# Performance work log

Measured on AMD Instinct MI355X. Metric: run time of the kernel, lower is better.

Reference implementation:

```python
import jax, jax.numpy as jnp
import numpy as np

T_V = 0.1
T_Q = 0.1
NEG_VIDEO_IOU = 0.5
POS_VIDEO_TOPK = 1
MARGIN = 0.0
EPS = 1e-12


def _normalize(x):
    # F.normalize(dim=-1) with eps clamp
    n = jnp.linalg.norm(x, axis=-1, keepdims=True)
    return x / jnp.maximum(n, EPS)


def _log_cross_entropy(pos_score, all_score, neg_mask, t, m):
    pos_exp = jnp.exp((pos_score - m) / t)
    neg_exp_sum = jnp.sum(jnp.exp(all_score / t) * neg_mask, axis=-1)
    loss = -((pos_score - m) / t - jnp.log(pos_exp + neg_exp_sum))
    return jnp.mean(loss)


def setup_inputs() -> dict:
    B, C, N, S = 32, 256, 64, 64
    key = jax.random.key(0)
    k1, k2, k3 = jax.random.split(key, 3)
    video_feats = jax.random.normal(k1, (B, C, N, N), dtype=jnp.float32)
    sents_feats = jax.random.normal(k2, (S, C), dtype=jnp.float32)
    iou2ds = jax.random.uniform(k3, (S, N, N), dtype=jnp.float32)
    mask2d = jnp.triu(jnp.ones((N, N), dtype=bool))  # P = N*(N+1)/2 = 2080
    num_targets = jnp.full((B,), S // B, dtype=jnp.int32)  # sums to S
    return {"video_feats": video_feats, "sents_feats": sents_feats,
            "num_targets": num_targets, "iou2ds": iou2ds, "mask2d": mask2d}


def reference(video_feats, sents_feats, num_targets, iou2ds, mask2d):
    B, C, N, _ = video_feats.shape
    S = sents_feats.shape[0]
    K = POS_VIDEO_TOPK
    # mask2d / num_targets are structural constants -> resolve on host
    flat_idx = np.nonzero(np.asarray(mask2d).reshape(-1))[0]   # [P]
    P = flat_idx.shape[0]
    scatter_idx = np.repeat(np.arange(B), np.asarray(num_targets))  # [S]

    # masked_select of valid proposals
    vf = video_feats.reshape(B, C, N * N)[:, :, flat_idx]      # [B,C,P]
    vf = jnp.transpose(vf, (0, 2, 1))                          # [B,P,C]
    iou = iou2ds.reshape(S, N * N)[:, flat_idx]                # [S,P]

    vf = _normalize(vf)
    sf = _normalize(sents_feats)                               # [S,C]

    # top-k proposals per sentence
    topk_idx = jax.lax.top_k(iou, K)[1]                        # [S,K]
    sv = vf[scatter_idx]                                       # [S,P,C]
    topk_video = jnp.take_along_axis(sv, topk_idx[:, :, None], axis=1)  # [S,K,C]

    # inter-video loss
    inter_video_pos = jnp.einsum('skc,sc->sk', topk_video, sf)          # [S,K]
    inter_video_all = jnp.einsum('skc,tc->skt', topk_video, sf)         # [S,K,S]
    inter_video_neg_mask = (~jnp.eye(S, dtype=bool))[:, None, :]        # [S,1,S]
    loss_inter_video = _log_cross_entropy(
        inter_video_pos, inter_video_all, inter_video_neg_mask, T_V, MARGIN)

    # inter-query loss
    inter_query_all = jnp.einsum('sc,bpc->sbp', sf, vf).reshape(S, 1, B * P)
    same_video = jnp.asarray(scatter_idx)[:, None] == jnp.arange(B)[None, :]  # [S,B]
    pos_mask = same_video[:, :, None] & (iou > NEG_VIDEO_IOU)[:, None, :]     # [S,B,P]
    inter_query_neg_mask = (~pos_mask).reshape(S, 1, B * P)
    loss_inter_query = _log_cross_entropy(
        inter_video_pos, inter_query_all, inter_query_neg_mask, T_Q, MARGIN)

    return (loss_inter_video, loss_inter_query)
```

## Files before the change

### kernel.cpp

```cpp
#include <hip/hip_runtime.h>
#include <hip/hip_bf16.h>
#include <math.h>

constexpr int B_ = 32;
constexpr int C_ = 256;
constexpr int N_ = 64;
constexpr int S_ = 64;
constexpr int NPIX = N_ * N_;
constexpr int QB = B_ * N_;

#define T_V_INV 10.0f
#define T_Q_INV 10.0f
#define NEG_IOU 0.5f

typedef __attribute__((ext_vector_type(8))) short short8;
typedef __attribute__((ext_vector_type(4))) float f32x4;

static __device__ __forceinline__ unsigned short f2bf(float x) {
  __hip_bfloat16 h = __float2bfloat16(x);
  unsigned short u;
  __builtin_memcpy(&u, &h, sizeof(u));
  return u;
}

__global__ __launch_bounds__(256) void k_setup(
    const float* __restrict__ sents, const float* __restrict__ iou,
    const int* __restrict__ nt,
    float* __restrict__ sf_t, unsigned short* __restrict__ sf_frag,
    int* __restrict__ scatter, int* __restrict__ top_pix) {
  int bid = blockIdx.x, tid = threadIdx.x;
  __shared__ float wsum[4];
  __shared__ float bval[256];
  __shared__ int bidx[256];

  if (bid < S_) {
    int s = bid, c = tid;
    float v = sents[s * C_ + c];
    float ss = v * v;
    #pragma unroll
    for (int o = 32; o; o >>= 1) ss += __shfl_xor(ss, o);
    if ((c & 63) == 0) wsum[c >> 6] = ss;
    __syncthreads();
    float tot = wsum[0] + wsum[1] + wsum[2] + wsum[3];
    float rn = 1.0f / fmaxf(sqrtf(tot), 1e-12f);
    float o = v * rn;
    sf_t[c * S_ + s] = o;
    int ks = c >> 5, q = (c >> 3) & 3, j = c & 7;
    int mt = s >> 4, m = s & 15;
    sf_frag[((ks * 4 + mt) * 64 + (q * 16 + m)) * 8 + j] = f2bf(o);

    float bv = -1.0f;
    int bi = 0x7fffffff;
    for (int pix = tid; pix < NPIX; pix += 256) {
      int r = pix >> 6, c0 = pix & 63;
      if (c0 >= r) {
        float x = iou[s * NPIX + pix];
        if (x > bv) { bv = x; bi = pix; }
      }
    }
    bval[tid] = bv; bidx[tid] = bi;
    __syncthreads();
    for (int st = 128; st; st >>= 1) {
      if (tid < st) {
        float ov = bval[tid + st]; int oi = bidx[tid + st];
        if (ov > bval[tid] || (ov == bval[tid] && oi < bidx[tid])) {
          bval[tid] = ov; bidx[tid] = oi;
        }
      }
      __syncthreads();
    }
    if (tid == 0) top_pix[s] = bidx[0];
  } else {
    if (tid < S_) {
      int cum = 0, res = 0;
      for (int b = 0; b < B_; b++) {
        int nb = nt[b];
        if (tid >= cum && tid < cum + nb) res = b;
        cum += nb;
      }
      scatter[tid] = res;
    }
  }
}

__global__ __launch_bounds__(256) void k_main(
    const float* __restrict__ V, const float* __restrict__ iou,
    const short8* __restrict__ Afrag, const float* __restrict__ sf_t,
    const int* __restrict__ scatter, const int* __restrict__ top_pix,
    float* __restrict__ partials, float* __restrict__ pos_score,
    float* __restrict__ loss_vid) {
  __shared__ int ssc[S_];
  __shared__ float part[4][S_];
  __shared__ float vh[C_];
  __shared__ float red[4];
  __shared__ float pdm[4][S_];

  int tid = threadIdx.x;

  if (blockIdx.x < QB) {
    if (tid < S_) ssc[tid] = scatter[tid];
    __syncthreads();

    int b = blockIdx.x >> 6, r = blockIdx.x & 63;
    int w = tid >> 6, lane = tid & 63;
    int n = lane & 15, q = lane >> 4;
    int col = w * 16 + n;
    int pix = r * 64 + col;
    bool active = (col >= r);

    const float* vb = V + (size_t)b * C_ * NPIX + pix;
    f32x4 acc[4] = {f32x4{0,0,0,0}, f32x4{0,0,0,0}, f32x4{0,0,0,0}, f32x4{0,0,0,0}};
    float ssq = 0.0f;

    for (int ks = 0; ks < 8; ks++) {
      short8 bfrag;
      #pragma unroll
      for (int j = 0; j < 8; j++) {
        int c = ks * 32 + q * 8 + j;
        float v = active ? vb[(size_t)c * NPIX] : 0.0f;
        ssq = fmaf(v, v, ssq);
        bfrag[j] = (short)f2bf(v);
      }
      #pragma unroll
      for (int mt = 0; mt < 4; mt++) {
        short8 a = Afrag[(ks * 4 + mt) * 64 + lane];
        acc[mt] = __builtin_amdgcn_mfma_f32_16x16x32_bf16(a, bfrag, acc[mt], 0, 0, 0);
      }
    }

    ssq += __shfl_xor(ssq, 16);
    ssq += __shfl_xor(ssq, 32);
    float rs = T_Q_INV / fmaxf(sqrtf(ssq), 1e-12f);

    #pragma unroll
    for (int mt = 0; mt < 4; mt++) {
      #pragma unroll
      for (int rr = 0; rr < 4; rr++) {
        int s = mt * 16 + q * 4 + rr;
        float e = active ? __expf(acc[mt][rr] * rs) : 0.0f;
        if (active && ssc[s] == b) {
          if (iou[s * NPIX + pix] > NEG_IOU) e = 0.0f;
        }
        e += __shfl_xor(e, 1);
        e += __shfl_xor(e, 2);
        e += __shfl_xor(e, 4);
        e += __shfl_xor(e, 8);
        if (n == 0) part[w][s] = e;
      }
    }
    __syncthreads();
    if (tid < S_) {
      partials[(size_t)blockIdx.x * S_ + tid] =
          part[0][tid] + part[1][tid] + part[2][tid] + part[3][tid];
    }
  } else {
    int s = blockIdx.x - QB;
    int b = scatter[s];
    int pix = top_pix[s];
    float v = V[((size_t)b * C_ + tid) * NPIX + pix];
    float ss = v * v;
    #pragma unroll
    for (int o = 32; o; o >>= 1) ss += __shfl_xor(ss, o);
    if ((tid & 63) == 0) red[tid >> 6] = ss;
    __syncthreads();
    float tot = red[0] + red[1] + red[2] + red[3];
    float rn = 1.0f / fmaxf(sqrtf(tot), 1e-12f);
    vh[tid] = v * rn;
    __syncthreads();
    int so = tid & 63, chunk = tid >> 6;
    float pd = 0.0f;
    #pragma unroll 8
    for (int c = chunk * 64; c < chunk * 64 + 64; c++)
      pd = fmaf(vh[c], sf_t[c * S_ + so], pd);
    pdm[chunk][so] = pd;
    __syncthreads();
    if (tid < S_) {
      float dot = pdm[0][tid] + pdm[1][tid] + pdm[2][tid] + pdm[3][tid];
      if (tid == s) pos_score[s] = dot;
      float pos = __shfl(dot, s);
      float e = (tid == s) ? 0.0f : __expf(dot * T_V_INV);
      #pragma unroll
      for (int o = 32; o; o >>= 1) e += __shfl_xor(e, o);
      if (tid == 0) {
        float pp = pos * T_V_INV;
        loss_vid[s] = -(pp - logf(__expf(pp) + e));
      }
    }
  }
}

__global__ __launch_bounds__(1024) void k_tail(
    const float* __restrict__ partials, const float* __restrict__ pos_score,
    const float* __restrict__ loss_vid, float* __restrict__ out) {
  int tid = threadIdx.x;
  int s = tid & 63, g = tid >> 6;
  __shared__ float m[16][S_];
  float acc = 0.0f;
  for (int blk = g; blk < QB; blk += 16) acc += partials[(size_t)blk * S_ + s];
  m[g][s] = acc;
  __syncthreads();
  if (tid < S_) {
    float neg = 0.0f;
    #pragma unroll
    for (int gg = 0; gg < 16; gg++) neg += m[gg][tid];
    float p = pos_score[tid] * T_Q_INV;
    float lq = -(p - logf(__expf(p) + neg));
    float lv = loss_vid[tid];
    #pragma unroll
    for (int o = 32; o; o >>= 1) {
      lq += __shfl_xor(lq, o);
      lv += __shfl_xor(lv, o);
    }
    if (tid == 0) {
      out[0] = lv / (float)S_;
      out[1] = lq / (float)S_;
    }
  }
}

extern "C" void kernel_launch(void* const* d_in, const int* in_sizes, int n_in,
                              void* d_out, int out_size, void* d_ws, size_t ws_size,
                              hipStream_t stream) {
  const float* V     = (const float*)d_in[0];
  const float* sents = (const float*)d_in[1];
  const int*   nt    = (const int*)d_in[2];
  const float* iou   = (const float*)d_in[3];

  float* ws = (float*)d_ws;
  float*          sf_t    = ws;
  unsigned short* sf_frag = (unsigned short*)(ws + 16384);
  int*   scatter   = (int*)(ws + 16384 + 8192);
  int*   top_pix   = scatter + S_;
  float* pos_score = (float*)(top_pix + S_);
  float* loss_vid  = pos_score + S_;
  float* partials  = loss_vid + S_;

  k_setup<<<S_ + 1, 256, 0, stream>>>(sents, iou, nt, sf_t, sf_frag, scatter, top_pix);
  k_main <<<QB + S_, 256, 0, stream>>>(V, iou, (const short8*)sf_frag, sf_t,
                                       scatter, top_pix, partials, pos_score, loss_vid);
  k_tail <<<1, 1024, 0, stream>>>(partials, pos_score, loss_vid, (float*)d_out);
}
```

Before: 249.5 us.

## Fuse tail reduction into main kernel via atomics and last-block finalize

Removes the separate tail kernel. Per-block partial sums now go into eight striped atomic accumulators, and a global counter lets the last block compute the final losses. The top-k video blocks are moved to the front of the grid so they are scheduled early. This drops one kernel launch and the 2048x64 partials round trip, at the cost of atomic contention on a small buffer and a nondeterministic float summation order.

After: 306.3 us. +22.8%, slower.

```diff
diff --git a/kernel.cpp b/kernel.cpp
--- a/kernel.cpp
+++ b/kernel.cpp
@@ -8,6 +8,8 @@
 constexpr int S_ = 64;
 constexpr int NPIX = N_ * N_;
 constexpr int QB = B_ * N_;
+constexpr int TOTAL_BLOCKS = S_ + QB;
+constexpr int NACC = 8;
 
 #define T_V_INV 10.0f
 #define T_Q_INV 10.0f
@@ -27,7 +29,9 @@
     const float* __restrict__ sents, const float* __restrict__ iou,
     const int* __restrict__ nt,
     float* __restrict__ sf_t, unsigned short* __restrict__ sf_frag,
-    int* __restrict__ scatter, int* __restrict__ top_pix) {
+    int* __restrict__ scatter, int* __restrict__ top_pix,
+    float* __restrict__ neg_acc, float* __restrict__ pos_score,
+    float* __restrict__ loss_vid, unsigned int* __restrict__ counter) {
   int bid = blockIdx.x, tid = threadIdx.x;
   __shared__ float wsum[4];
   __shared__ float bval[256];
@@ -80,6 +84,10 @@
       }
       scatter[tid] = res;
     }
+    for (int i = tid; i < NACC * S_; i += 256) neg_acc[i] = 0.0f;
+    if (tid >= 64 && tid < 128) pos_score[tid - 64] = 0.0f;
+    if (tid >= 128 && tid < 192) loss_vid[tid - 128] = 0.0f;
+    if (tid == 0) *counter = 0u;
   }
 }
 
@@ -87,21 +95,24 @@
     const float* __restrict__ V, const float* __restrict__ iou,
     const short8* __restrict__ Afrag, const float* __restrict__ sf_t,
     const int* __restrict__ scatter, const int* __restrict__ top_pix,
-    float* __restrict__ partials, float* __restrict__ pos_score,
-    float* __restrict__ loss_vid) {
+    float* __restrict__ neg_acc, float* __restrict__ pos_score,
+    float* __restrict__ loss_vid, unsigned int* __restrict__ counter,
+    float* __restrict__ out) {
   __shared__ int ssc[S_];
   __shared__ float part[4][S_];
   __shared__ float vh[C_];
   __shared__ float red[4];
   __shared__ float pdm[4][S_];
+  __shared__ int sIsLast;
 
   int tid = threadIdx.x;
 
-  if (blockIdx.x < QB) {
+  if (blockIdx.x >= S_) {
     if (tid < S_) ssc[tid] = scatter[tid];
     __syncthreads();
 
-    int b = blockIdx.x >> 6, r = blockIdx.x & 63;
+    int qb = blockIdx.x - S_;
+    int b = qb >> 6, r = qb & 63;
     int w = tid >> 6, lane = tid & 63;
     int n = lane & 15, q = lane >> 4;
     int col = w * 16 + n;
@@ -150,11 +161,11 @@
     }
     __syncthreads();
     if (tid < S_) {
-      partials[(size_t)blockIdx.x * S_ + tid] =
-          part[0][tid] + part[1][tid] + part[2][tid] + part[3][tid];
+      float v = part[0][tid] + part[1][tid] + part[2][tid] + part[3][tid];
+      atomicAdd(&neg_acc[(qb & (NACC - 1)) * S_ + tid], v);
     }
   } else {
-    int s = blockIdx.x - QB;
+    int s = blockIdx.x;
     int b = scatter[s];
     int pix = top_pix[s];
     float v = V[((size_t)b * C_ + tid) * NPIX + pix];
@@ -176,44 +187,45 @@
     __syncthreads();
     if (tid < S_) {
       float dot = pdm[0][tid] + pdm[1][tid] + pdm[2][tid] + pdm[3][tid];
-      if (tid == s) pos_score[s] = dot;
+      if (tid == s) atomicAdd(&pos_score[s], dot);
       float pos = __shfl(dot, s);
       float e = (tid == s) ? 0.0f : __expf(dot * T_V_INV);
       #pragma unroll
       for (int o = 32; o; o >>= 1) e += __shfl_xor(e, o);
       if (tid == 0) {
         float pp = pos * T_V_INV;
-        loss_vid[s] = -(pp - logf(__expf(pp) + e));
-      }
-    }
-  }
-}
-
-__global__ __launch_bounds__(1024) void k_tail(
-    const float* __restrict__ partials, const float* __restrict__ pos_score,
-    const float* __restrict__ loss_vid, float* __restrict__ out) {
-  int tid = threadIdx.x;
-  int s = tid & 63, g = tid >> 6;
-  __shared__ float m[16][S_];
-  float acc = 0.0f;
-  for (int blk = g; blk < QB; blk += 16) acc += partials[(size_t)blk * S_ + s];
-  m[g][s] = acc;
+        atomicAdd(&loss_vid[s], -(pp - logf(__expf(pp) + e)));
+      }
+    }
+  }
+
   __syncthreads();
-  if (tid < S_) {
-    float neg = 0.0f;
-    #pragma unroll
-    for (int gg = 0; gg < 16; gg++) neg += m[gg][tid];
-    float p = pos_score[tid] * T_Q_INV;
-    float lq = -(p - logf(__expf(p) + neg));
-    float lv = loss_vid[tid];
-    #pragma unroll
-    for (int o = 32; o; o >>= 1) {
-      lq += __shfl_xor(lq, o);
-      lv += __shfl_xor(lv, o);
-    }
-    if (tid == 0) {
-      out[0] = lv / (float)S_;
-      out[1] = lq / (float)S_;
+  if (tid == 0) {
+    __threadfence();
+    unsigned int old = atomicAdd(counter, 1u);
+    sIsLast = (old == (unsigned int)(TOTAL_BLOCKS - 1));
+  }
+  __syncthreads();
+  if (sIsLast) {
+    __threadfence();
+    if (tid < S_) {
+      float neg = 0.0f;
+      #pragma unroll
+      for (int k = 0; k < NACC; k++)
+        neg += atomicAdd(&neg_acc[k * S_ + tid], 0.0f);
+      float ps = atomicAdd(&pos_score[tid], 0.0f);
+      float lv = atomicAdd(&loss_vid[tid], 0.0f);
+      float p = ps * T_Q_INV;
+      float lq = -(p - logf(__expf(p) + neg));
+      #pragma unroll
+      for (int o = 32; o; o >>= 1) {
+        lq += __shfl_xor(lq, o);
+        lv += __shfl_xor(lv, o);
+      }
+      if (tid == 0) {
+        out[0] = lv / (float)S_;
+        out[1] = lq / (float)S_;
+      }
     }
   }
 }
@@ -233,10 +245,14 @@
   int*   top_pix   = scatter + S_;
   float* pos_score = (float*)(top_pix + S_);
   float* loss_vid  = pos_score + S_;
-  float* partials  = loss_vid + S_;
-
-  k_setup<<<S_ + 1, 256, 0, stream>>>(sents, iou, nt, sf_t, sf_frag, scatter, top_pix);
-  k_main <<<QB + S_, 256, 0, stream>>>(V, iou, (const short8*)sf_frag, sf_t,
-                                       scatter, top_pix, partials, pos_score, loss_vid);
-  k_tail <<<1, 1024, 0, stream>>>(partials, pos_score, loss_vid, (float*)d_out);
-}
+  float* neg_acc   = loss_vid + S_;
+  unsigned int* counter = (unsigned int*)(neg_acc + NACC * S_);
+
+  k_setup<<<S_ + 1, 256, 0, stream>>>(sents, iou, nt, sf_t, sf_frag, scatter,
+                                      top_pix, neg_acc, pos_score, loss_vid,
+                                      counter);
+  k_main <<<TOTAL_BLOCKS, 256, 0, stream>>>(V, iou, (const short8*)sf_frag,
+                                            sf_t, scatter, top_pix, neg_acc,
+                                            pos_score, loss_vid, counter,
+                                            (float*)d_out);
+}
```
